# Optimization experiments

Hardware: AMD Instinct MI355X
Metric: run time of the kernel (lower is better)

## Reference

```python
import jax, jax.numpy as jnp
import numpy as np


def setup_inputs() -> dict:
    key = jax.random.key(0)
    kq, kk, kv, km, kb = jax.random.split(key, 5)
    B, H, S, D = 4, 16, 2048, 64
    Q = jax.random.normal(kq, (B, H, S, D), dtype=jnp.float32)
    K = jax.random.normal(kk, (B, H, S, D), dtype=jnp.float32)
    V = jax.random.normal(kv, (B, H, S, D), dtype=jnp.float32)
    # key-padding style mask, broadcasts over query dim; 0 -> masked
    mask = jax.random.randint(km, (B, 1, 1, S), 0, 2, dtype=jnp.int32)
    attn_bias = jax.random.normal(kb, (1, H, S, S), dtype=jnp.float32)
    return {"Q": Q, "K": K, "V": V, "mask": mask, "attn_bias": attn_bias}


def reference(Q, K, V, mask, attn_bias):
    d_k = Q.shape[-1]
    scale = 1.0 / jnp.sqrt(jnp.asarray(d_k, Q.dtype))
    # [B,H,Sq,Sk] scores
    scores = jnp.einsum("bhqd,bhkd->bhqk", Q, K) * scale
    scores = scores + attn_bias
    scores = jnp.where(mask == 0, jnp.asarray(-1e9, scores.dtype), scores)
    attn = jax.nn.softmax(scores, axis=-1)
    # dropout is identity in eval/reference mode
    output = jnp.einsum("bhqk,bhkd->bhqd", attn, V)
    return output, attn
```

## Files before the change

### kernel.cpp

```cpp
#include <hip/hip_runtime.h>

#define NB 4
#define NH 16
#define NS 2048
#define ND 64

typedef __attribute__((ext_vector_type(8))) short short8;
typedef __attribute__((ext_vector_type(4))) float floatx4;
typedef __attribute__((ext_vector_type(4))) int intx4;
typedef __attribute__((ext_vector_type(4))) unsigned uintx4;

#define MFMA __builtin_amdgcn_mfma_f32_16x16x32_bf16
#define WAITV(N) asm volatile("s_waitcnt vmcnt(" #N ")" ::: "memory")
#define WAITL asm volatile("s_waitcnt lgkmcnt(0)" ::: "memory")

__device__ __forceinline__ unsigned short f2bf(float f) {
  unsigned u = __builtin_bit_cast(unsigned, f);
  u = (u + 0x7FFFu + ((u >> 16) & 1u)) >> 16;
  return (unsigned short)u;
}
__device__ __forceinline__ float bf2f(unsigned u16) {
  unsigned u = u16 << 16;
  return __builtin_bit_cast(float, u);
}
__device__ __forceinline__ void gload16(const void* g, void* l) {
  __builtin_amdgcn_global_load_lds(
      (const __attribute__((address_space(1))) unsigned int*)g,
      (__attribute__((address_space(3))) unsigned int*)l, 16, 0, 0);
}

__global__ __launch_bounds__(256) void prep_k_kernel(const float* __restrict__ K,
                                                     unsigned short* __restrict__ kb) {
  size_t i = ((size_t)blockIdx.x * 256 + threadIdx.x) * 4;
  floatx4 v = *(const floatx4*)(K + i);
  unsigned long long o = 0;
  o |= (unsigned long long)f2bf(v[0]);
  o |= (unsigned long long)f2bf(v[1]) << 16;
  o |= (unsigned long long)f2bf(v[2]) << 32;
  o |= (unsigned long long)f2bf(v[3]) << 48;
  *(unsigned long long*)(kb + i) = o;
}

__global__ __launch_bounds__(256) void prep_vt_kernel(const float* __restrict__ V,
                                                      unsigned short* __restrict__ vt) {
  __shared__ float tile[64][65];
  int kc = blockIdx.x & 31;
  int bh = blockIdx.x >> 5;
  int k0 = kc * 64;
  const float* src = V + ((size_t)bh * NS + k0) * ND;
  int t = threadIdx.x;
  int r0 = t >> 4;
  int c = (t & 15) * 4;
  for (int rr = 0; rr < 4; ++rr) {
    int r = rr * 16 + r0;
    floatx4 v = *(const floatx4*)(src + (size_t)r * ND + c);
    tile[r][c + 0] = v[0]; tile[r][c + 1] = v[1];
    tile[r][c + 2] = v[2]; tile[r][c + 3] = v[3];
  }
  __syncthreads();
  unsigned short* dst = vt + (size_t)bh * ND * NS + k0;
  for (int i = 0; i < 16; ++i) {
    int lin = i * 256 + t;
    int d = lin >> 6, k = lin & 63;
    dst[(size_t)d * NS + k] = f2bf(tile[k][d]);
  }
}

__global__ __launch_bounds__(256) void prep_mask_kernel(const int* __restrict__ mask,
                                                        unsigned* __restrict__ mb) {
  int t = blockIdx.x * 256 + threadIdx.x;
  const int* mp = mask + t * 32;
  unsigned w = 0;
#pragma unroll
  for (int i = 0; i < 32; ++i) w |= (mp[i] != 0 ? 1u : 0u) << i;
  mb[t] = w;
}

__global__ void __attribute__((amdgpu_flat_work_group_size(256, 256),
                               amdgpu_waves_per_eu(3, 4)))
attn_kernel(
    const float* __restrict__ Q,
    const unsigned short* __restrict__ Kb,
    const unsigned short* __restrict__ VT,
    const unsigned* __restrict__ maskbits,
    const float* __restrict__ bias,
    float* __restrict__ out,
    float* __restrict__ attn) {
  extern __shared__ char smem[];

  const int bid0 = blockIdx.x;
  const int bid = (bid0 & 7) * 1024 + (bid0 >> 3);
  const int b = bid & 3;
  const int qt = (bid >> 2) & 127;
  const int h = bid >> 9;
  const int q0 = qt * 16;

  const int tid = threadIdx.x;
  const int wave = tid >> 6;
  const int lane = tid & 63;
  const int lg = lane >> 4;
  const int lc = lane & 15;
  const int lg4 = lg * 4;
  const int lg8 = lg * 8;
  const size_t bh = (size_t)(b * NH + h);

  char* smStage = smem + wave * 12288;
  float* sums = (float*)(smem + 49152);

  short8 aq0, aq1;
  {
    const float* qrow = Q + (bh * NS + (size_t)(q0 + lc)) * ND + lg8;
    floatx4 f0 = *(const floatx4*)(qrow);
    floatx4 f1 = *(const floatx4*)(qrow + 4);
    floatx4 f2 = *(const floatx4*)(qrow + 32);
    floatx4 f3 = *(const floatx4*)(qrow + 36);
#pragma unroll
    for (int j = 0; j < 4; ++j) {
      aq0[j] = (short)f2bf(f0[j] * 0.125f);
      aq0[4 + j] = (short)f2bf(f1[j] * 0.125f);
      aq1[j] = (short)f2bf(f2[j] * 0.125f);
      aq1[4 + j] = (short)f2bf(f3[j] * 0.125f);
    }
  }
  const int ksb = wave * 512;
  intx4 mva, mvb, mvc, mvd;
  {
    const intx4* mp = (const intx4*)(maskbits + b * (NS / 32) + wave * 16);
    mva = mp[0]; mvb = mp[1]; mvc = mp[2]; mvd = mp[3];
  }

  const int kj = (lane & 7) ^ (lane >> 3);
  const unsigned short* kRowPtr = Kb + bh * NS * ND + (size_t)(lane >> 3) * ND + kj * 8;
  const float* bRowPtr = bias + ((size_t)h * NS + (size_t)(q0 + (lane >> 3))) * NS + kj * 4;
  const int vj = (lane & 3) ^ ((lane >> 2) & 3);
  const unsigned short* vRowPtr = VT + bh * (size_t)ND * NS + (size_t)(lane >> 2) * NS + vj * 8;

  const int lc128 = lc * 128;
  const int kRd0 = ((lg ^ (lc & 7)) * 16);
  const int kRd1 = (((4 + lg) ^ (lc & 7)) * 16);
  const int vRd = ((lg ^ (lc & 3)) * 16);

  const bool lo_half = (lg < 2);
  const bool sndR = (lg == 0) || (lg == 3);
  float psum = 0.f;

  asm volatile("s_waitcnt vmcnt(0)" ::: "memory");

#define KISSUE(IT, SLOT) {                                                \
    const int k0_ = ksb + (IT) * 32;                                      \
    const unsigned short* ks_ = kRowPtr + (size_t)k0_ * ND;               \
    char* kd_ = smStage + (SLOT) * 4096;                                  \
    gload16(ks_, kd_);                                                    \
    gload16(ks_ + 8 * ND, kd_ + 1024);                                    \
    gload16(ks_ + 16 * ND, kd_ + 2048);                                   \
    gload16(ks_ + 24 * ND, kd_ + 3072);                                   \
    const float* bs_ = bRowPtr + k0_;                                     \
    char* bd_ = smStage + 8192 + (SLOT) * 2048;                           \
    gload16(bs_, bd_);                                                    \
    gload16(bs_ + 8 * NS, bd_ + 1024);                                    \
  }

#define SUBTILE(IT, SLOT, NW, MW)                                         \
  uintx4 pw##IT;                                                          \
  {                                                                       \
    WAITV(NW);                                                            \
    const char* kb_ = smStage + (SLOT) * 4096;                            \
    const char* bb_ = smStage + 8192 + (SLOT) * 2048;                     \
    short8 kA0 = *(const short8*)(kb_ + lc128 + kRd0);                    \
    short8 kB0 = *(const short8*)(kb_ + lc128 + kRd1);                    \
    short8 kA1 = *(const short8*)(kb_ + 2048 + lc128 + kRd0);             \
    short8 kB1 = *(const short8*)(kb_ + 2048 + lc128 + kRd1);             \
    floatx4 bV0 = *(const floatx4*)(bb_ + lc128 + kRd0);                  \
    floatx4 bV1 = *(const floatx4*)(bb_ + lc128 + kRd1);                  \
    unsigned uA0, uA1, uB0, uB1;                                          \
    {                                                                     \
      floatx4 c = bV0;                                                    \
      c = MFMA(kA0, aq0, c, 0, 0, 0);                                     \
      c = MFMA(kB0, aq1, c, 0, 0, 0);                                     \
      unsigned mb_ = (MW) >> lg4;                                         \
      float p0 = (mb_ & 1u) ? __expf(c[0]) : 0.f;                         \
      float p1 = (mb_ & 2u) ? __expf(c[1]) : 0.f;                         \
      float p2 = (mb_ & 4u) ? __expf(c[2]) : 0.f;                         \
      float p3 = (mb_ & 8u) ? __expf(c[3]) : 0.f;                         \
      psum += (p0 + p1) + (p2 + p3);                                      \
      uA0 = (unsigned)f2bf(p0) | ((unsigned)f2bf(p1) << 16);              \
      uA1 = (unsigned)f2bf(p2) | ((unsigned)f2bf(p3) << 16);              \
    }                                                                     \
    {                                                                     \
      floatx4 c = bV1;                                                    \
      c = MFMA(kA1, aq0, c, 0, 0, 0);                                     \
      c = MFMA(kB1, aq1, c, 0, 0, 0);                                     \
      unsigned mb_ = (MW) >> (16 + lg4);                                  \
      float p0 = (mb_ & 1u) ? __expf(c[0]) : 0.f;                         \
      float p1 = (mb_ & 2u) ? __expf(c[1]) : 0.f;                         \
      float p2 = (mb_ & 4u) ? __expf(c[2]) : 0.f;                         \
      float p3 = (mb_ & 8u) ? __expf(c[3]) : 0.f;                         \
      psum += (p0 + p1) + (p2 + p3);                                      \
      uB0 = (unsigned)f2bf(p0) | ((unsigned)f2bf(p1) << 16);              \
      uB1 = (unsigned)f2bf(p2) | ((unsigned)f2bf(p3) << 16);              \
    }                                                                     \
    unsigned ma = lo_half ? uA0 : uB0;                                    \
    unsigned mb2 = lo_half ? uA1 : uB1;                                   \
    unsigned sa = lo_half ? uB0 : uA0;                                    \
    unsigned sb = lo_half ? uB1 : uA1;                                    \
    unsigned r1a = __shfl_xor(sa, 32);                                    \
    unsigned r1b = __shfl_xor(sb, 32);                                    \
    unsigned s2a = sndR ? r1a : ma;                                       \
    unsigned s2b = sndR ? r1b : mb2;                                      \
    unsigned g2a = __shfl_xor(s2a, 16);                                   \
    unsigned g2b = __shfl_xor(s2b, 16);                                   \
    pw##IT[0] = (lg == 0) ? ma : (lg == 2) ? r1a : g2a;                   \
    pw##IT[1] = (lg == 0) ? mb2 : (lg == 2) ? r1b : g2b;                  \
    pw##IT[2] = (lg == 1) ? r1a : (lg == 3) ? ma : g2a;                   \
    pw##IT[3] = (lg == 1) ? r1b : (lg == 3) ? mb2 : g2b;                  \
    WAITL;                                                                \
  }

  KISSUE(0, 0) KISSUE(1, 1)
  SUBTILE(0, 0, 6, mva[0])  KISSUE(2, 0)
  SUBTILE(1, 1, 6, mva[1])  KISSUE(3, 1)
  SUBTILE(2, 0, 6, mva[2])  KISSUE(4, 0)
  SUBTILE(3, 1, 6, mva[3])  KISSUE(5, 1)
  SUBTILE(4, 0, 6, mvb[0])  KISSUE(6, 0)
  SUBTILE(5, 1, 6, mvb[1])  KISSUE(7, 1)
  SUBTILE(6, 0, 6, mvb[2])  KISSUE(8, 0)
  SUBTILE(7, 1, 6, mvb[3])  KISSUE(9, 1)
  SUBTILE(8, 0, 6, mvc[0])  KISSUE(10, 0)
  SUBTILE(9, 1, 6, mvc[1])  KISSUE(11, 1)
  SUBTILE(10, 0, 6, mvc[2]) KISSUE(12, 0)
  SUBTILE(11, 1, 6, mvc[3]) KISSUE(13, 1)
  SUBTILE(12, 0, 6, mvd[0]) KISSUE(14, 0)
  SUBTILE(13, 1, 6, mvd[1]) KISSUE(15, 1)
  SUBTILE(14, 0, 6, mvd[2])
  SUBTILE(15, 1, 0, mvd[3])
#undef SUBTILE
#undef KISSUE

#define VISSUE(W, SLOT) {                                                 \
    const int kk_ = ksb + (W) * 32;                                       \
    const unsigned short* vs_ = vRowPtr + kk_;                            \
    char* vd_ = smStage + (SLOT) * 4096;                                  \
    gload16(vs_, vd_);                                                    \
    gload16(vs_ + 16 * NS, vd_ + 1024);                                   \
    gload16(vs_ + 32 * NS, vd_ + 2048);                                   \
    gload16(vs_ + 48 * NS, vd_ + 3072);                                   \
  }

  psum += __shfl_xor(psum, 16);
  psum += __shfl_xor(psum, 32);
  if (lane < 16) sums[wave * 16 + lane] = psum;
  VISSUE(0, 0) VISSUE(1, 1)
  WAITL;
  __builtin_amdgcn_sched_barrier(0);
  __builtin_amdgcn_s_barrier();
  __builtin_amdgcn_sched_barrier(0);
  float inv;
  {
    float t = sums[0 * 16 + lc] + sums[1 * 16 + lc] + sums[2 * 16 + lc] + sums[3 * 16 + lc];
    inv = 1.f / t;
  }

  floatx4 o0 = {0.f, 0.f, 0.f, 0.f}, o1 = {0.f, 0.f, 0.f, 0.f};
  floatx4 o2 = {0.f, 0.f, 0.f, 0.f}, o3 = {0.f, 0.f, 0.f, 0.f};

#define PVWIN(W, SLOT, NW) {                                              \
    WAITV(NW);                                                            \
    const char* vb_ = smStage + (SLOT) * 4096;                            \
    short8 vb0 = *(const short8*)(vb_ + (0 * 16 + lc) * 64 + vRd);        \
    short8 vb1 = *(const short8*)(vb_ + (1 * 16 + lc) * 64 + vRd);        \
    short8 vb2 = *(const short8*)(vb_ + (2 * 16 + lc) * 64 + vRd);        \
    short8 vb3 = *(const short8*)(vb_ + (3 * 16 + lc) * 64 + vRd);        \
    short8 pa = __builtin_bit_cast(short8, pw##W);                        \
    o0 = MFMA(pa, vb0, o0, 0, 0, 0);                                      \
    o1 = MFMA(pa, vb1, o1, 0, 0, 0);                                      \
    o2 = MFMA(pa, vb2, o2, 0, 0, 0);                                      \
    o3 = MFMA(pa, vb3, o3, 0, 0, 0);                                      \
    WAITL;                                                                \
  }

  PVWIN(0, 0, 4)   VISSUE(2, 0)
  PVWIN(1, 1, 4)   VISSUE(3, 1)
  PVWIN(2, 0, 4)   VISSUE(4, 0)
  PVWIN(3, 1, 4)   VISSUE(5, 1)
  PVWIN(4, 0, 4)   VISSUE(6, 0)
  PVWIN(5, 1, 4)   VISSUE(7, 1)
  PVWIN(6, 0, 4)   VISSUE(8, 0)
  PVWIN(7, 1, 4)   VISSUE(9, 1)
  PVWIN(8, 0, 4)   VISSUE(10, 0)
  PVWIN(9, 1, 4)   VISSUE(11, 1)
  PVWIN(10, 0, 4)  VISSUE(12, 0)
  PVWIN(11, 1, 4)  VISSUE(13, 1)
  PVWIN(12, 0, 4)  VISSUE(14, 0)
  PVWIN(13, 1, 4)  VISSUE(15, 1)
  PVWIN(14, 0, 4)
  PVWIN(15, 1, 0)
#undef PVWIN
#undef VISSUE

  {
    float* arow = attn + (bh * NS + (size_t)(q0 + lc)) * NS + lg8;
#define STW(W) {                                                          \
    const int kk_ = ksb + (W) * 32;                                       \
    floatx4 fa, fb;                                                       \
    fa[0] = bf2f(pw##W[0] & 0xffffu) * inv;                               \
    fa[1] = bf2f(pw##W[0] >> 16) * inv;                                   \
    fa[2] = bf2f(pw##W[1] & 0xffffu) * inv;                               \
    fa[3] = bf2f(pw##W[1] >> 16) * inv;                                   \
    fb[0] = bf2f(pw##W[2] & 0xffffu) * inv;                               \
    fb[1] = bf2f(pw##W[2] >> 16) * inv;                                   \
    fb[2] = bf2f(pw##W[3] & 0xffffu) * inv;                               \
    fb[3] = bf2f(pw##W[3] >> 16) * inv;                                   \
    __builtin_nontemporal_store(fa, (floatx4*)(arow + kk_));              \
    __builtin_nontemporal_store(fb, (floatx4*)(arow + kk_ + 4));          \
  }
    STW(0)  STW(1)  STW(2)  STW(3)  STW(4)  STW(5)  STW(6)  STW(7)
    STW(8)  STW(9)  STW(10) STW(11) STW(12) STW(13) STW(14) STW(15)
#undef STW
  }

  __builtin_amdgcn_sched_barrier(0);
  __builtin_amdgcn_s_barrier();
  __builtin_amdgcn_sched_barrier(0);
  float (*Ored)[16][72] = (float (*)[16][72])smem;
#pragma unroll
  for (int r = 0; r < 4; ++r) {
    Ored[wave][lg4 + r][0 * 16 + lc] = o0[r];
    Ored[wave][lg4 + r][1 * 16 + lc] = o1[r];
    Ored[wave][lg4 + r][2 * 16 + lc] = o2[r];
    Ored[wave][lg4 + r][3 * 16 + lc] = o3[r];
  }
  WAITL;
  __builtin_amdgcn_sched_barrier(0);
  __builtin_amdgcn_s_barrier();
  __builtin_amdgcn_sched_barrier(0);
  {
    const int q = tid >> 4;
    const int c4 = (tid & 15) * 4;
    floatx4 acc = {0.f, 0.f, 0.f, 0.f};
#pragma unroll
    for (int w = 0; w < 4; ++w) acc += *(const floatx4*)&Ored[w][q][c4];
    float tot = sums[0 * 16 + q] + sums[1 * 16 + q] + sums[2 * 16 + q] + sums[3 * 16 + q];
    const float invq = 1.f / tot;
    floatx4 res;
    res[0] = acc[0] * invq; res[1] = acc[1] * invq;
    res[2] = acc[2] * invq; res[3] = acc[3] * invq;
    __builtin_nontemporal_store(res, (floatx4*)(out + (bh * NS + (size_t)(q0 + q)) * ND + c4));
  }
}

extern "C" void kernel_launch(void* const* d_in, const int* in_sizes, int n_in,
                              void* d_out, int out_size, void* d_ws, size_t ws_size,
                              hipStream_t stream) {
  const float* Q = (const float*)d_in[0];
  const float* K = (const float*)d_in[1];
  const float* V = (const float*)d_in[2];
  const int* mask = (const int*)d_in[3];
  const float* bias = (const float*)d_in[4];

  float* out = (float*)d_out;
  float* attn = out + (size_t)NB * NH * NS * ND;

  unsigned short* kb = (unsigned short*)d_ws;
  unsigned short* vt = kb + (size_t)NB * NH * NS * ND;
  unsigned* mb = (unsigned*)(vt + (size_t)NB * NH * NS * ND);

  const int lds_bytes = 4 * 12288 + 4 * 16 * 4;
  prep_k_kernel<<<(NB * NH * NS * ND) / (256 * 4), 256, 0, stream>>>(K, kb);
  prep_vt_kernel<<<NB * NH * (NS / 64), 256, 0, stream>>>(V, vt);
  prep_mask_kernel<<<1, 256, 0, stream>>>(mask, mb);
  attn_kernel<<<NB * NH * (NS / 16), 256, lds_bytes, stream>>>(Q, kb, vt, mb, bias, out, attn);
}
```

Baseline: 668.2 us.

## Load attention bias directly into registers instead of staging through LDS

The bias tile is now fetched with inline-asm global_load_dwordx4 straight into MFMA accumulator layout registers, triple-buffered in registers, rather than copied into LDS and read back. This shrinks per-wave LDS staging from 12 KB to 8 KB, which may allow more blocks per CU, and removes the LDS round trip for bias. Wait counts and sched barriers were adjusted to track the extra in-flight loads. The attn output stores also switch from nontemporal to regular stores. The risks are higher register pressure and fragile hand-counted vmcnt values.

Result: slower. 725.9 us (+8.6%).

```diff
diff --git a/kernel.cpp b/kernel.cpp
--- a/kernel.cpp
+++ b/kernel.cpp
@@ -104,8 +104,8 @@
   const int lg8 = lg * 8;
   const size_t bh = (size_t)(b * NH + h);
 
-  char* smStage = smem + wave * 12288;
-  float* sums = (float*)(smem + 49152);
+  char* smStage = smem + wave * 8192;
+  float* sums = (float*)(smem + 32768);
 
   short8 aq0, aq1;
   {
@@ -131,9 +131,9 @@
 
   const int kj = (lane & 7) ^ (lane >> 3);
   const unsigned short* kRowPtr = Kb + bh * NS * ND + (size_t)(lane >> 3) * ND + kj * 8;
-  const float* bRowPtr = bias + ((size_t)h * NS + (size_t)(q0 + (lane >> 3))) * NS + kj * 4;
   const int vj = (lane & 3) ^ ((lane >> 2) & 3);
   const unsigned short* vRowPtr = VT + bh * (size_t)ND * NS + (size_t)(lane >> 2) * NS + vj * 8;
+  const float* bp0 = bias + ((size_t)h * NS + (size_t)(q0 + lc)) * NS + lg4;
 
   const int lc128 = lc * 128;
   const int kRd0 = ((lg ^ (lc & 7)) * 16);
@@ -145,6 +145,16 @@
   float psum = 0.f;
 
   asm volatile("s_waitcnt vmcnt(0)" ::: "memory");
+
+  floatx4 bA0, bB0, bA1, bB1, bA2, bB2;
+
+#define BISS(I, S)                                                        \
+  asm volatile("global_load_dwordx4 %0, %2, off\n\t"                      \
+               "global_load_dwordx4 %1, %3, off"                          \
+               : "=&v"(bA##S), "=&v"(bB##S)                               \
+               : "v"(bp0 + (size_t)(ksb + (I) * 32)),                     \
+                 "v"(bp0 + (size_t)(ksb + (I) * 32 + 16))                 \
+               : "memory");
 
 #define KISSUE(IT, SLOT) {                                                \
     const int k0_ = ksb + (IT) * 32;                                      \
@@ -154,27 +164,21 @@
     gload16(ks_ + 8 * ND, kd_ + 1024);                                    \
     gload16(ks_ + 16 * ND, kd_ + 2048);                                   \
     gload16(ks_ + 24 * ND, kd_ + 3072);                                   \
-    const float* bs_ = bRowPtr + k0_;                                     \
-    char* bd_ = smStage + 8192 + (SLOT) * 2048;                           \
-    gload16(bs_, bd_);                                                    \
-    gload16(bs_ + 8 * NS, bd_ + 1024);                                    \
-  }
-
-#define SUBTILE(IT, SLOT, NW, MW)                                         \
+  }
+
+#define SUBTILE(IT, KS, BS, NW, MW)                                       \
   uintx4 pw##IT;                                                          \
   {                                                                       \
     WAITV(NW);                                                            \
-    const char* kb_ = smStage + (SLOT) * 4096;                            \
-    const char* bb_ = smStage + 8192 + (SLOT) * 2048;                     \
+    __builtin_amdgcn_sched_barrier(0);                                    \
+    const char* kb_ = smStage + (KS) * 4096;                              \
     short8 kA0 = *(const short8*)(kb_ + lc128 + kRd0);                    \
     short8 kB0 = *(const short8*)(kb_ + lc128 + kRd1);                    \
     short8 kA1 = *(const short8*)(kb_ + 2048 + lc128 + kRd0);             \
     short8 kB1 = *(const short8*)(kb_ + 2048 + lc128 + kRd1);             \
-    floatx4 bV0 = *(const floatx4*)(bb_ + lc128 + kRd0);                  \
-    floatx4 bV1 = *(const floatx4*)(bb_ + lc128 + kRd1);                  \
     unsigned uA0, uA1, uB0, uB1;                                          \
     {                                                                     \
-      floatx4 c = bV0;                                                    \
+      floatx4 c = bA##BS;                                                 \
       c = MFMA(kA0, aq0, c, 0, 0, 0);                                     \
       c = MFMA(kB0, aq1, c, 0, 0, 0);                                     \
       unsigned mb_ = (MW) >> lg4;                                         \
@@ -187,7 +191,7 @@
       uA1 = (unsigned)f2bf(p2) | ((unsigned)f2bf(p3) << 16);              \
     }                                                                     \
     {                                                                     \
-      floatx4 c = bV1;                                                    \
+      floatx4 c = bB##BS;                                                 \
       c = MFMA(kA1, aq0, c, 0, 0, 0);                                     \
       c = MFMA(kB1, aq1, c, 0, 0, 0);                                     \
       unsigned mb_ = (MW) >> (16 + lg4);                                  \
@@ -216,25 +220,27 @@
     WAITL;                                                                \
   }
 
+  BISS(0, 0) BISS(1, 1) BISS(2, 2)
   KISSUE(0, 0) KISSUE(1, 1)
-  SUBTILE(0, 0, 6, mva[0])  KISSUE(2, 0)
-  SUBTILE(1, 1, 6, mva[1])  KISSUE(3, 1)
-  SUBTILE(2, 0, 6, mva[2])  KISSUE(4, 0)
-  SUBTILE(3, 1, 6, mva[3])  KISSUE(5, 1)
-  SUBTILE(4, 0, 6, mvb[0])  KISSUE(6, 0)
-  SUBTILE(5, 1, 6, mvb[1])  KISSUE(7, 1)
-  SUBTILE(6, 0, 6, mvb[2])  KISSUE(8, 0)
-  SUBTILE(7, 1, 6, mvb[3])  KISSUE(9, 1)
-  SUBTILE(8, 0, 6, mvc[0])  KISSUE(10, 0)
-  SUBTILE(9, 1, 6, mvc[1])  KISSUE(11, 1)
-  SUBTILE(10, 0, 6, mvc[2]) KISSUE(12, 0)
-  SUBTILE(11, 1, 6, mvc[3]) KISSUE(13, 1)
-  SUBTILE(12, 0, 6, mvd[0]) KISSUE(14, 0)
-  SUBTILE(13, 1, 6, mvd[1]) KISSUE(15, 1)
-  SUBTILE(14, 0, 6, mvd[2])
-  SUBTILE(15, 1, 0, mvd[3])
+  SUBTILE(0, 0, 0, 4, mva[0])   BISS(3, 0)  KISSUE(2, 0)
+  SUBTILE(1, 1, 1, 6, mva[1])   BISS(4, 1)  KISSUE(3, 1)
+  SUBTILE(2, 0, 2, 6, mva[2])   BISS(5, 2)  KISSUE(4, 0)
+  SUBTILE(3, 1, 0, 6, mva[3])   BISS(6, 0)  KISSUE(5, 1)
+  SUBTILE(4, 0, 1, 6, mvb[0])   BISS(7, 1)  KISSUE(6, 0)
+  SUBTILE(5, 1, 2, 6, mvb[1])   BISS(8, 2)  KISSUE(7, 1)
+  SUBTILE(6, 0, 0, 6, mvb[2])   BISS(9, 0)  KISSUE(8, 0)
+  SUBTILE(7, 1, 1, 6, mvb[3])   BISS(10, 1) KISSUE(9, 1)
+  SUBTILE(8, 0, 2, 6, mvc[0])   BISS(11, 2) KISSUE(10, 0)
+  SUBTILE(9, 1, 0, 6, mvc[1])   BISS(12, 0) KISSUE(11, 1)
+  SUBTILE(10, 0, 1, 6, mvc[2])  BISS(13, 1) KISSUE(12, 0)
+  SUBTILE(11, 1, 2, 6, mvc[3])  BISS(14, 2) KISSUE(13, 1)
+  SUBTILE(12, 0, 0, 6, mvd[0])  BISS(15, 0) KISSUE(14, 0)
+  SUBTILE(13, 1, 1, 6, mvd[1])              KISSUE(15, 1)
+  SUBTILE(14, 0, 2, 4, mvd[2])
+  SUBTILE(15, 1, 0, 0, mvd[3])
 #undef SUBTILE
 #undef KISSUE
+#undef BISS
 
 #define VISSUE(W, SLOT) {                                                 \
     const int kk_ = ksb + (W) * 32;                                       \
@@ -265,6 +271,7 @@
 
 #define PVWIN(W, SLOT, NW) {                                              \
     WAITV(NW);                                                            \
+    __builtin_amdgcn_sched_barrier(0);                                    \
     const char* vb_ = smStage + (SLOT) * 4096;                            \
     short8 vb0 = *(const short8*)(vb_ + (0 * 16 + lc) * 64 + vRd);        \
     short8 vb1 = *(const short8*)(vb_ + (1 * 16 + lc) * 64 + vRd);        \
@@ -310,8 +317,8 @@
     fb[1] = bf2f(pw##W[2] >> 16) * inv;                                   \
     fb[2] = bf2f(pw##W[3] & 0xffffu) * inv;                               \
     fb[3] = bf2f(pw##W[3] >> 16) * inv;                                   \
-    __builtin_nontemporal_store(fa, (floatx4*)(arow + kk_));              \
-    __builtin_nontemporal_store(fb, (floatx4*)(arow + kk_ + 4));          \
+    *(floatx4*)(arow + kk_) = fa;                                         \
+    *(floatx4*)(arow + kk_ + 4) = fb;                                     \
   }
     STW(0)  STW(1)  STW(2)  STW(3)  STW(4)  STW(5)  STW(6)  STW(7)
     STW(8)  STW(9)  STW(10) STW(11) STW(12) STW(13) STW(14) STW(15)
@@ -364,7 +371,7 @@
   unsigned short* vt = kb + (size_t)NB * NH * NS * ND;
   unsigned* mb = (unsigned*)(vt + (size_t)NB * NH * NS * ND);
 
-  const int lds_bytes = 4 * 12288 + 4 * 16 * 4;
+  const int lds_bytes = 4 * 8192 + 4 * 16 * 4;
   prep_k_kernel<<<(NB * NH * NS * ND) / (256 * 4), 256, 0, stream>>>(K, kb);
   prep_vt_kernel<<<NB * NH * (NS / 64), 256, 0, stream>>>(V, vt);
   prep_mask_kernel<<<1, 256, 0, stream>>>(mask, mb);
```
